# Optimization experiments

Measured on AMD Instinct MI355X. Metric: run time of the kernel, lower is better.

Reference implementation:

```python
import jax, jax.numpy as jnp
import numpy as np

B, N, D = 8, 8192, 512
WS = 128          # ATTENTION_WINDOW_SIZE
LB = 1            # ATTENTION_WINDOW_LOOKBACK (look_backward)
NW = N // WS      # number of windows (N divisible by WS -> autopad no-op)


def setup_inputs() -> dict:
    key = jax.random.key(0)
    ks = jax.random.split(key, 4)
    s = 0.02
    return {
        "x": jax.random.normal(ks[0], (B, N, D), dtype=jnp.float32),
        "w_q": jax.random.normal(ks[1], (D, D), dtype=jnp.float32) * s,
        "b_q": jnp.zeros((D,), dtype=jnp.float32),
        "w_k": jax.random.normal(ks[2], (D, D), dtype=jnp.float32) * s,
        "b_k": jnp.zeros((D,), dtype=jnp.float32),
        "w_v": jax.random.normal(ks[3], (D, D), dtype=jnp.float32) * s,
        "b_v": jnp.zeros((D,), dtype=jnp.float32),
    }


def _look_around(t, pad_value):
    # t: (B, NW, WS, ...) -> concat of [backward..current] windows along window-length axis
    pad_width = [(0, 0), (LB, 0)] + [(0, 0)] * (t.ndim - 2)
    padded = jnp.pad(t, pad_width, constant_values=pad_value)
    return jnp.concatenate([padded[:, i:i + NW] for i in range(LB + 1)], axis=2)


def _local_attention(q, k, v):
    scale = D ** -0.5
    bq = q.reshape(B, NW, WS, D)
    bk = _look_around(k.reshape(B, NW, WS, D), 0.0)   # (B, NW, (LB+1)*WS, D)
    bv = _look_around(v.reshape(B, NW, WS, D), 0.0)

    # absolute position ticks for causal + padding masks
    tq = jnp.arange(N).reshape(1, NW, WS)                               # query positions
    tk = _look_around(jnp.arange(N).reshape(1, NW, WS), -1)             # key positions, -1 = pad

    sim = jnp.einsum('bwie,bwje->bwij', bq, bk) * scale                 # (B, NW, WS, (LB+1)*WS)
    mask = (tq[..., :, None] < tk[..., None, :]) | (tk[..., None, :] < 0)
    sim = jnp.where(mask, -jnp.finfo(sim.dtype).max, sim)
    attn = jax.nn.softmax(sim, axis=-1)                                  # dropout = 0 -> no-op
    out = jnp.einsum('bwij,bwje->bwie', attn, bv)
    return out.reshape(B, N, D)


def reference(x, w_q, b_q, w_k, b_k, w_v, b_v):
    q = x @ w_q.T + b_q
    k = x @ w_k.T + b_k
    v = x @ w_v.T + b_v
    return _local_attention(q, k, v)
```

## Files before the change

kernel.cpp:

```cpp
#include <hip/hip_runtime.h>


typedef __bf16 bf16x8 __attribute__((ext_vector_type(8)));
typedef float f32x4 __attribute__((ext_vector_type(4)));
typedef unsigned short u16x8 __attribute__((ext_vector_type(8)));

#define BATCH 8
#define SEQ   8192
#define DIM   512
#define NWIN  64
#define TOKS  (BATCH * SEQ)
#define WSELEM ((size_t)TOKS * DIM)

__device__ __forceinline__ unsigned short f2b(float f) {
    union { float f; unsigned int u; } c; c.f = f;
    unsigned int u = c.u;
    return (unsigned short)((u + 0x7FFFu + ((u >> 16) & 1u)) >> 16);
}

__device__ __forceinline__ int swz64(int row, int col) {
    return (row * 64 + col) ^ ((row & 7) << 3);
}

__device__ __forceinline__ void gload_lds16(const unsigned short* g,
                                            unsigned short* l) {
    __builtin_amdgcn_global_load_lds(
        (const __attribute__((address_space(1))) void*)g,
        (__attribute__((address_space(3))) void*)l, 16, 0, 0);
}

__global__ __launch_bounds__(256) void k_cvt(const float* __restrict__ s,
                                             unsigned short* __restrict__ d,
                                             int n8) {
    const int stride = gridDim.x * blockDim.x;
    for (int i = blockIdx.x * blockDim.x + threadIdx.x; i < n8; i += stride) {
        const float4 a = ((const float4*)s)[2 * i];
        const float4 b = ((const float4*)s)[2 * i + 1];
        u16x8 v;
        v[0] = f2b(a.x); v[1] = f2b(a.y); v[2] = f2b(a.z); v[3] = f2b(a.w);
        v[4] = f2b(b.x); v[5] = f2b(b.y); v[6] = f2b(b.z); v[7] = f2b(b.w);
        ((u16x8*)d)[i] = v;
    }
}

__global__ __launch_bounds__(256, 2) void k_qkv(
    const unsigned short* __restrict__ xb, const unsigned short* __restrict__ wb,
    const float* __restrict__ bq, const float* __restrict__ bk,
    const float* __restrict__ bv,
    unsigned short* __restrict__ qo, unsigned short* __restrict__ ko,
    unsigned short* __restrict__ vto)
{
    __shared__ __align__(16) unsigned short sm[32768];
    unsigned short* Xs = sm;

    int bid = (int)blockIdx.x;
    bid = (bid & 7) * 256 + (bid >> 3);
    const int mt = bid >> 2, nt = bid & 3;
    const int rbase = mt << 7;
    const int cbase = nt << 7;

    const unsigned short* __restrict__ xsrc0 = xb + ((size_t)rbase << 9);
    const unsigned short* __restrict__ wsrc0 = wb + ((size_t)cbase << 9);

    const int tid  = threadIdx.x;
    const int lane = tid & 63;
    const int wid  = tid >> 6;
    const int wm = wid >> 1, wn = wid & 1;
    const int l15 = lane & 15, lg = lane >> 4;

    f32x4 acc[3][4][4];
#pragma unroll
    for (int s = 0; s < 3; ++s)
#pragma unroll
        for (int m = 0; m < 4; ++m)
#pragma unroll
            for (int n = 0; n < 4; ++n) acc[s][m][n] = (f32x4){0.f, 0.f, 0.f, 0.f};

    const int srow = tid >> 3;
    const int gs   = ((tid & 7) ^ (srow & 7)) << 3;
    const int ldso = tid << 3;

    for (int ks = 0; ks < 8; ++ks) {
        const int kc = ks << 6;
#pragma unroll
        for (int i = 0; i < 4; ++i) {
            const int row = (i << 5) + srow;
            gload_lds16(xsrc0 + ((size_t)row << 9) + kc + gs, Xs + (i << 11) + ldso);
        }
#pragma unroll
        for (int ws = 0; ws < 3; ++ws) {
#pragma unroll
            for (int i = 0; i < 4; ++i) {
                const int row = (i << 5) + srow;
                gload_lds16(wsrc0 + ((size_t)ws << 18) + ((size_t)row << 9) + kc + gs,
                            sm + 8192 + (ws << 13) + (i << 11) + ldso);
            }
        }
        __syncthreads();
#pragma unroll
        for (int kk = 0; kk < 64; kk += 32) {
            const int cu = kk + (lg << 3);
            bf16x8 af[4];
#pragma unroll
            for (int m = 0; m < 4; ++m)
                af[m] = *(const bf16x8*)&Xs[swz64((wm << 6) + (m << 4) + l15, cu)];
#pragma unroll
            for (int ws = 0; ws < 3; ++ws) {
                const unsigned short* Wsb = sm + 8192 + (ws << 13);
                bf16x8 bfr[4];
#pragma unroll
                for (int n = 0; n < 4; ++n)
                    bfr[n] = *(const bf16x8*)&Wsb[swz64((wn << 6) + (n << 4) + l15, cu)];
#pragma unroll
                for (int m = 0; m < 4; ++m)
#pragma unroll
                    for (int n = 0; n < 4; ++n)
                        acc[ws][m][n] = __builtin_amdgcn_mfma_f32_16x16x32_bf16(
                            af[m], bfr[n], acc[ws][m][n], 0, 0, 0);
            }
        }
        __syncthreads();
    }

#pragma unroll
    for (int ws = 0; ws < 2; ++ws) {
        unsigned short* __restrict__ out = ws ? ko : qo;
        const float* __restrict__ bias = ws ? bk : bq;
#pragma unroll
        for (int n = 0; n < 4; ++n) {
            const int col = cbase + (wn << 6) + (n << 4) + l15;
            const float bv_ = bias[col];
#pragma unroll
            for (int m = 0; m < 4; ++m)
#pragma unroll
                for (int j = 0; j < 4; ++j) {
                    const int row = rbase + (wm << 6) + (m << 4) + (lg << 2) + j;
                    out[(size_t)row * DIM + col] = f2b(acc[ws][m][n][j] + bv_);
                }
        }
    }
#pragma unroll
    for (int n = 0; n < 4; ++n) {
        const int dv = (wn << 6) + (n << 4) + l15;
        const float bv_ = bv[cbase + dv];
#pragma unroll
        for (int m = 0; m < 4; ++m)
#pragma unroll
            for (int j = 0; j < 4; ++j) {
                const int tok = (wm << 6) + (m << 4) + (lg << 2) + j;
                sm[tok * 129 + dv] = f2b(acc[2][m][n][j] + bv_);
            }
    }
    __syncthreads();
    {
        const int batch = rbase >> 13;
        const int ntok  = rbase & 8191;
        const int dvl0  = tid >> 4;
        const int t16   = (tid & 15) << 3;
#pragma unroll
        for (int p = 0; p < 8; ++p) {
            const int dvl = (p << 4) + dvl0;
            u16x8 v;
#pragma unroll
            for (int j = 0; j < 8; ++j) v[j] = sm[(t16 + j) * 129 + dvl];
            const int key0 = ntok + t16;
            *(u16x8*)&vto[(((size_t)(batch * 256 + (key0 >> 5)) << 9)
                           + (size_t)(cbase + dvl)) * 32 + (key0 & 31)] = v;
        }
    }
}

__global__ __launch_bounds__(512, 2) void k_attn(
    const unsigned short* __restrict__ q,
    const unsigned short* __restrict__ k,
    const unsigned short* __restrict__ vt3,
    float* __restrict__ out)
{
    __shared__ __align__(16) unsigned short Kb[32768];
    __shared__ __align__(16) unsigned short Pl[32768];

    int bid = (int)blockIdx.x;
    bid = (bid & 7) * 64 + (bid >> 3);
    const int b = bid >> 6, w = bid & 63;
    const int tid  = threadIdx.x;
    const int lane = tid & 63, wid = tid >> 6;
    const int l15 = lane & 15, lg = lane >> 4;
    const int kstart = (w - 1) << 7;
    const size_t qrow0 = ((size_t)b << 13) + ((size_t)w << 7);
    const size_t kbase = (size_t)b << 13;

    const int srow = tid >> 3;
    const int s0   = tid & 7;

    f32x4 acc[16];
#pragma unroll
    for (int n = 0; n < 16; ++n) acc[n] = (f32x4){0.f, 0.f, 0.f, 0.f};

    auto stageK = [&](int buf, int ds) {
#pragma unroll
        for (int i = 0; i < 4; ++i) {
            const int r = (i << 6) + srow;
            int krow = kstart + r; krow = krow < 0 ? 0 : krow;
            gload_lds16(k + (kbase + krow) * DIM + (ds << 6) + ((s0 ^ (r & 7)) << 3),
                        Kb + (buf << 14) + (i << 12) + (tid << 3));
        }
    };

    stageK(0, 0);
    stageK(1, 1);
    __syncthreads();
    for (int ds = 0; ds < 8; ++ds) {
        const unsigned short* Kc = Kb + ((ds & 1) << 14);
#pragma unroll
        for (int kk2 = 0; kk2 < 2; ++kk2) {
            const int cu = (kk2 << 5) + (lg << 3);
            const bf16x8 af = *(const bf16x8*)
                &q[(qrow0 + (wid << 4) + l15) * DIM + (ds << 6) + cu];
#pragma unroll
            for (int n = 0; n < 16; ++n) {
                const bf16x8 bf = *(const bf16x8*)&Kc[swz64((n << 4) + l15, cu)];
                acc[n] = __builtin_amdgcn_mfma_f32_16x16x32_bf16(af, bf, acc[n], 0, 0, 0);
            }
        }
        __syncthreads();
        if (ds + 2 < 8) stageK(ds & 1, ds + 2);
    }

    const int c5base = kstart >> 5;
    auto stageV = [&](int buf, int kk) {
        int c5 = c5base + kk; c5 = c5 < 0 ? 0 : c5;
        const unsigned short* src = vt3 + ((size_t)(b * 256 + c5) << 14);
#pragma unroll
        for (int i = 0; i < 4; ++i)
            gload_lds16(src + (i << 12) + (tid << 3),
                        Kb + (buf << 14) + (i << 12) + (tid << 3));
    };
    stageV(0, 0);
    stageV(1, 1);

    const float scale = 0.04419417382415922f;
    float inv[4];
    unsigned short* Pw = Pl + (wid << 12);
#pragma unroll
    for (int jj = 0; jj < 4; ++jj) {
        const int r  = (lg << 2) + jj;
        const int qr = (wid << 4) + r;
        float mx = -3.0e38f;
#pragma unroll
        for (int n = 0; n < 16; ++n) {
            const int c = (n << 4) + l15;
            const bool keep = (c <= qr + 128) && (w > 0 || c >= 128);
            const float s = keep ? acc[n][jj] * scale : -INFINITY;
            acc[n][jj] = s;
            mx = fmaxf(mx, s);
        }
#pragma unroll
        for (int o = 1; o < 16; o <<= 1) mx = fmaxf(mx, __shfl_xor(mx, o));
        float sum = 0.f;
#pragma unroll
        for (int n = 0; n < 16; ++n) {
            const float p = __expf(acc[n][jj] - mx);
            acc[n][jj] = p;
            sum += p;
        }
#pragma unroll
        for (int o = 1; o < 16; o <<= 1) sum += __shfl_xor(sum, o);
        inv[jj] = 1.0f / sum;
#pragma unroll
        for (int n = 0; n < 16; ++n) {
            const int c = (n << 4) + l15;
            Pw[(r << 8) + ((((c >> 3) ^ r) << 3) | (c & 7))] = f2b(acc[n][jj]);
        }
    }
    __syncthreads();

    f32x4 oacc[32];
#pragma unroll
    for (int n = 0; n < 32; ++n) oacc[n] = (f32x4){0.f, 0.f, 0.f, 0.f};

    for (int kk = 0; kk < 8; ++kk) {
        const unsigned short* Vc = Kb + ((kk & 1) << 14);
        const bf16x8 pa = *(const bf16x8*)
            &Pw[(l15 << 8) + ((((kk << 2) + lg) ^ l15) << 3)];
#pragma unroll
        for (int n = 0; n < 32; ++n) {
            const bf16x8 bv_ = *(const bf16x8*)&Vc[(((n << 4) + l15) << 5) + (lg << 3)];
            oacc[n] = __builtin_amdgcn_mfma_f32_16x16x32_bf16(pa, bv_, oacc[n], 0, 0, 0);
        }
        if (kk < 7) {
            __syncthreads();
            if (kk + 2 < 8) stageV(kk & 1, kk + 2);
        }
    }

#pragma unroll
    for (int n = 0; n < 32; ++n) {
        const int dv = (n << 4) + l15;
        float* orow = out + (qrow0 + (wid << 4) + (lg << 2)) * DIM + dv;
#pragma unroll
        for (int jj = 0; jj < 4; ++jj)
            orow[(size_t)jj * DIM] = oacc[n][jj] * inv[jj];
    }
}

extern "C" void kernel_launch(void* const* d_in, const int* in_sizes, int n_in,
                              void* d_out, int out_size, void* d_ws, size_t ws_size,
                              hipStream_t stream) {
    (void)in_sizes; (void)n_in; (void)out_size; (void)ws_size;
    const float* x  = (const float*)d_in[0];
    const float* wq = (const float*)d_in[1];
    const float* bq = (const float*)d_in[2];
    const float* wk = (const float*)d_in[3];
    const float* bk = (const float*)d_in[4];
    const float* wv = (const float*)d_in[5];
    const float* bv = (const float*)d_in[6];
    float* out = (float*)d_out;

    unsigned short* qws  = (unsigned short*)d_ws;
    unsigned short* kws  = qws + WSELEM;
    unsigned short* vtws = kws + WSELEM;

    unsigned short* xbuf = (unsigned short*)d_out;
    unsigned short* wbuf = xbuf + WSELEM;

    k_cvt<<<2048, 256, 0, stream>>>(x, xbuf, (int)(WSELEM / 8));
    k_cvt<<<128, 256, 0, stream>>>(wq, wbuf, DIM * DIM / 8);
    k_cvt<<<128, 256, 0, stream>>>(wk, wbuf + DIM * DIM, DIM * DIM / 8);
    k_cvt<<<128, 256, 0, stream>>>(wv, wbuf + 2 * DIM * DIM, DIM * DIM / 8);
    k_qkv<<<2048, 256, 0, stream>>>(xbuf, wbuf, bq, bk, bv, qws, kws, vtws);
    k_attn<<<512, 512, 0, stream>>>(qws, kws, vtws, out);
}
```

Before: 238.5 us.

## Fuse fp32-to-bf16 conversion of x into the QKV projection GEMM

Drops the separate conversion kernel for x. The QKV GEMM now reads fp32 x straight into registers, converts to bf16, and writes it to swizzled LDS. The next k-step's x values are prefetched into registers after the barrier so the global loads overlap the MFMA work. The V-transpose store is also remapped so each wave writes contiguous 32-key chunks. The cost is that x is read as fp32 four times, once per column tile, plus higher register pressure from the prefetch buffer.

```diff
diff --git a/kernel.cpp b/kernel.cpp
--- a/kernel.cpp
+++ b/kernel.cpp
@@ -44,7 +44,7 @@
 }
 
 __global__ __launch_bounds__(256, 2) void k_qkv(
-    const unsigned short* __restrict__ xb, const unsigned short* __restrict__ wb,
+    const float* __restrict__ x, const unsigned short* __restrict__ wb,
     const float* __restrict__ bq, const float* __restrict__ bk,
     const float* __restrict__ bv,
     unsigned short* __restrict__ qo, unsigned short* __restrict__ ko,
@@ -59,7 +59,6 @@
     const int rbase = mt << 7;
     const int cbase = nt << 7;
 
-    const unsigned short* __restrict__ xsrc0 = xb + ((size_t)rbase << 9);
     const unsigned short* __restrict__ wsrc0 = wb + ((size_t)cbase << 9);
 
     const int tid  = threadIdx.x;
@@ -77,26 +76,51 @@
             for (int n = 0; n < 4; ++n) acc[s][m][n] = (f32x4){0.f, 0.f, 0.f, 0.f};
 
     const int srow = tid >> 3;
-    const int gs   = ((tid & 7) ^ (srow & 7)) << 3;
+    const int s0   = tid & 7;
+    const int xc   = s0 << 3;
+    const int gsw  = (s0 ^ (srow & 7)) << 3;
     const int ldso = tid << 3;
 
+    const float* xrp[4];
+    float4 xr[4][2];
+#pragma unroll
+    for (int i = 0; i < 4; ++i) {
+        xrp[i] = x + (size_t)(rbase + (i << 5) + srow) * DIM + xc;
+        xr[i][0] = *(const float4*)(xrp[i]);
+        xr[i][1] = *(const float4*)(xrp[i] + 4);
+    }
+
+#pragma unroll
     for (int ks = 0; ks < 8; ++ks) {
         const int kc = ks << 6;
 #pragma unroll
         for (int i = 0; i < 4; ++i) {
             const int row = (i << 5) + srow;
-            gload_lds16(xsrc0 + ((size_t)row << 9) + kc + gs, Xs + (i << 11) + ldso);
+            u16x8 v;
+            v[0] = f2b(xr[i][0].x); v[1] = f2b(xr[i][0].y);
+            v[2] = f2b(xr[i][0].z); v[3] = f2b(xr[i][0].w);
+            v[4] = f2b(xr[i][1].x); v[5] = f2b(xr[i][1].y);
+            v[6] = f2b(xr[i][1].z); v[7] = f2b(xr[i][1].w);
+            *(u16x8*)&Xs[swz64(row, xc)] = v;
         }
 #pragma unroll
         for (int ws = 0; ws < 3; ++ws) {
 #pragma unroll
             for (int i = 0; i < 4; ++i) {
                 const int row = (i << 5) + srow;
-                gload_lds16(wsrc0 + ((size_t)ws << 18) + ((size_t)row << 9) + kc + gs,
+                gload_lds16(wsrc0 + ((size_t)ws << 18) + ((size_t)row << 9) + kc + gsw,
                             sm + 8192 + (ws << 13) + (i << 11) + ldso);
             }
         }
         __syncthreads();
+        if (ks < 7) {
+            const int kn = (ks + 1) << 6;
+#pragma unroll
+            for (int i = 0; i < 4; ++i) {
+                xr[i][0] = *(const float4*)(xrp[i] + kn);
+                xr[i][1] = *(const float4*)(xrp[i] + kn + 4);
+            }
+        }
 #pragma unroll
         for (int kk = 0; kk < 64; kk += 32) {
             const int cu = kk + (lg << 3);
@@ -154,18 +178,18 @@
     __syncthreads();
     {
         const int batch = rbase >> 13;
-        const int ntok  = rbase & 8191;
-        const int dvl0  = tid >> 4;
-        const int t16   = (tid & 15) << 3;
-#pragma unroll
-        for (int p = 0; p < 8; ++p) {
-            const int dvl = (p << 4) + dvl0;
+        const int c5_0  = (rbase & 8191) >> 5;
+#pragma unroll
+        for (int s = 0; s < 8; ++s) {
+            const int c5sel = s & 3, dvh = s >> 2;
+            const int dvl  = (dvh << 6) + (wid << 4) + (lane >> 2);
+            const int keyo = (lane & 3) << 3;
+            const int tok0 = (c5sel << 5) + keyo;
             u16x8 v;
 #pragma unroll
-            for (int j = 0; j < 8; ++j) v[j] = sm[(t16 + j) * 129 + dvl];
-            const int key0 = ntok + t16;
-            *(u16x8*)&vto[(((size_t)(batch * 256 + (key0 >> 5)) << 9)
-                           + (size_t)(cbase + dvl)) * 32 + (key0 & 31)] = v;
+            for (int j = 0; j < 8; ++j) v[j] = sm[(tok0 + j) * 129 + dvl];
+            *(u16x8*)&vto[((size_t)((batch * 256 + c5_0 + c5sel) * 512
+                                    + cbase + dvl) << 5) + keyo] = v;
         }
     }
 }
@@ -320,13 +344,11 @@
     unsigned short* kws  = qws + WSELEM;
     unsigned short* vtws = kws + WSELEM;
 
-    unsigned short* xbuf = (unsigned short*)d_out;
-    unsigned short* wbuf = xbuf + WSELEM;
-
-    k_cvt<<<2048, 256, 0, stream>>>(x, xbuf, (int)(WSELEM / 8));
+    unsigned short* wbuf = (unsigned short*)d_out;
+
     k_cvt<<<128, 256, 0, stream>>>(wq, wbuf, DIM * DIM / 8);
     k_cvt<<<128, 256, 0, stream>>>(wk, wbuf + DIM * DIM, DIM * DIM / 8);
     k_cvt<<<128, 256, 0, stream>>>(wv, wbuf + 2 * DIM * DIM, DIM * DIM / 8);
-    k_qkv<<<2048, 256, 0, stream>>>(xbuf, wbuf, bq, bk, bv, qws, kws, vtws);
+    k_qkv<<<2048, 256, 0, stream>>>(x, wbuf, bq, bk, bv, qws, kws, vtws);
     k_attn<<<512, 512, 0, stream>>>(qws, kws, vtws, out);
 }
```

Measured after the change: 549.2 us. 2.3x slower.
